# Performance work log

Hardware: AMD Instinct MI355X
Metric: run time of the kernel (lower is better)

The kernel has to match this reference:

```python
import jax, jax.numpy as jnp
import numpy as np

N_NODES = 100000
N_EDGES = 1600000
IN_DIM = 256
OUT_DIM = 64


def setup_inputs() -> dict:
    key = jax.random.key(0)
    k1, k2, k3, k4, k5 = jax.random.split(key, 5)
    x = jax.random.normal(k1, (N_NODES, IN_DIM), dtype=jnp.float32)
    # glorot-ish small scales to keep the learned power exponent well-behaved
    W = jax.random.normal(k2, (IN_DIM, OUT_DIM), dtype=jnp.float32) * 0.05
    f_w = jax.random.normal(k3, (2 * OUT_DIM, 1), dtype=jnp.float32) * 0.05
    f_b = jnp.full((1,), 0.5, dtype=jnp.float32)  # constants([1], 0.5)
    row = jax.random.randint(k4, (N_EDGES,), 0, N_NODES, dtype=jnp.int64)
    col = jax.random.randint(k5, (N_EDGES,), 0, N_NODES, dtype=jnp.int64)
    return {"x": x, "W": W, "f_w": f_w, "f_b": f_b, "row": row, "col": col}


def reference(x, W, f_w, f_b, row, col):
    n = x.shape[0]
    pre_sup = x @ W                                   # [N, out]
    vi = pre_sup[row]                                 # [E, out] gather src
    vj = pre_sup[col]                                 # [E, out] gather dst
    # tiny edge MLP: score per edge
    s = jnp.concatenate([vi, vj], axis=1) @ f_w + f_b  # [E, 1]
    # degree = adjacency row-sum including self-loop (adj + I)
    deg = jax.ops.segment_sum(jnp.ones(row.shape[0], x.dtype), row,
                              num_segments=n) + 1.0    # [N]
    deg_vivj = (deg[row] * deg[col])[:, None]          # [E, 1]
    vals = jnp.power(deg_vivj, -s)[:, 0]               # [E] edge weights
    # sparse(support) @ pre_sup  ==  scatter-add over destination rows
    out = jax.ops.segment_sum(vals[:, None] * vj, row, num_segments=n)
    return jax.nn.relu(out)
```

## Files before the change

kernel.cpp:

```cpp
#include <hip/hip_runtime.h>

#define IN_DIM 256
#define OUT_DIM 64

typedef __attribute__((ext_vector_type(8))) short short8;
typedef __attribute__((ext_vector_type(4))) float frag_cd;

__device__ __forceinline__ unsigned short bf16_rne(float f) {
    unsigned u = __float_as_uint(f);
    u = (u + 0x7FFFu + ((u >> 16) & 1u)) >> 16;
    return (unsigned short)u;
}
__device__ __forceinline__ float bf16_to_f32(unsigned short h) {
    return __uint_as_float((unsigned)h << 16);
}

__global__ __launch_bounds__(256) void wprep_kernel(const float* __restrict__ W,
                                                    const float* __restrict__ f_w,
                                                    short8* __restrict__ wfrag,
                                                    float* __restrict__ wf0,
                                                    float* __restrict__ wf1) {
    const int t = threadIdx.x;
    float s0 = 0.f, s1 = 0.f;
    #pragma unroll 8
    for (int c = 0; c < 64; c++) {
        const float w = W[t * 64 + c];
        s0 += w * f_w[c];
        s1 += w * f_w[64 + c];
    }
    wf0[t] = s0;
    wf1[t] = s1;
    for (int e = t; e < 2048; e += 256) {
        const int lane = e & 63;
        const int ct = e >> 6;
        const int chunk = ct >> 2, tile = ct & 3;
        const int kb = chunk * 32 + ((lane >> 4) * 8);
        const int n = tile * 16 + (lane & 15);
        short8 f;
        #pragma unroll
        for (int j = 0; j < 8; j++)
            f[j] = (short)bf16_rne(W[(kb + j) * 64 + n]);
        wfrag[e] = f;
    }
}

__global__ __launch_bounds__(256) void gemm_rank_kernel(const float* __restrict__ x,
                                                        const short8* __restrict__ wfrag,
                                                        const float* __restrict__ wf0,
                                                        const float* __restrict__ wf1,
                                                        unsigned short* __restrict__ pre16,
                                                        float* __restrict__ a,
                                                        float2* __restrict__ bl,
                                                        const int* __restrict__ row,
                                                        unsigned* __restrict__ cnt,
                                                        unsigned* __restrict__ rank,
                                                        int N, int E,
                                                        int nblk_gemm, int nblk_rank, int G) {
    __shared__ short8 lds_wfrag[2048];
    __shared__ float4 lds_wf0[64];
    __shared__ float4 lds_wf1[64];
    const int r4 = blockIdx.x & 3;
    const int s = blockIdx.x >> 2;
    if (r4 != 3) {
        const int rb = s * 3 + r4;
        if (rb >= nblk_rank) return;
        const int i0 = rb * 1024 + threadIdx.x;
        const int i1 = i0 + 256, i2 = i0 + 512, i3 = i0 + 768;
        const bool v0 = i0 < E, v1 = i1 < E, v2 = i2 < E, v3 = i3 < E;
        unsigned rk0 = 0, rk1 = 0, rk2 = 0, rk3 = 0;
        if (v0) rk0 = atomicAdd(&cnt[row[i0]], 1u);
        if (v1) rk1 = atomicAdd(&cnt[row[i1]], 1u);
        if (v2) rk2 = atomicAdd(&cnt[row[i2]], 1u);
        if (v3) rk3 = atomicAdd(&cnt[row[i3]], 1u);
        if (rank) {
            if (v0) rank[i0] = rk0;
            if (v1) rank[i1] = rk1;
            if (v2) rank[i2] = rk2;
            if (v3) rank[i3] = rk3;
        }
        return;
    }
    const int g = s;
    if (g >= G) return;
    const int t = threadIdx.x;
    const int w = t >> 6;
    const int l = t & 63;
    const int m = l & 15;
    const int q = l >> 4;

    #pragma unroll
    for (int e = t; e < 2048; e += 256)
        ((int4*)lds_wfrag)[e] = ((const int4*)wfrag)[e];
    if (t < 64) lds_wf0[t] = ((const float4*)wf0)[t];
    else if (t < 128) lds_wf1[t - 64] = ((const float4*)wf1)[t - 64];
    __syncthreads();

    for (int tile = g; tile < nblk_gemm; tile += G) {
        const int row0 = tile * 64 + w * 16;
        const int arow = row0 + m;
        const int arowc = (arow < N) ? arow : (N - 1);
        const float* xr = x + (size_t)arowc * IN_DIM;

        float4 xv[16];
        #pragma unroll
        for (int c = 0; c < 8; c++) {
            xv[2 * c]     = *(const float4*)&xr[c * 32 + q * 8];
            xv[2 * c + 1] = *(const float4*)&xr[c * 32 + q * 8 + 4];
        }
        __builtin_amdgcn_sched_barrier(0);

        frag_cd acc0 = {0.f, 0.f, 0.f, 0.f};
        frag_cd acc1 = acc0, acc2 = acc0, acc3 = acc0;
        float ap = 0.f, bp = 0.f;

        #pragma unroll
        for (int c = 0; c < 8; c++) {
            const int k4 = c * 8 + q * 2;
            const float4 w0l = lds_wf0[k4];
            const float4 w0h = lds_wf0[k4 + 1];
            const float4 w1l = lds_wf1[k4];
            const float4 w1h = lds_wf1[k4 + 1];
            const short8 b0 = lds_wfrag[(c * 4 + 0) * 64 + l];
            const short8 b1 = lds_wfrag[(c * 4 + 1) * 64 + l];
            const short8 b2 = lds_wfrag[(c * 4 + 2) * 64 + l];
            const short8 b3 = lds_wfrag[(c * 4 + 3) * 64 + l];
            const float4 xl = xv[2 * c];
            const float4 xh = xv[2 * c + 1];

            ap += xl.x * w0l.x + xl.y * w0l.y + xl.z * w0l.z + xl.w * w0l.w
                + xh.x * w0h.x + xh.y * w0h.y + xh.z * w0h.z + xh.w * w0h.w;
            bp += xl.x * w1l.x + xl.y * w1l.y + xl.z * w1l.z + xl.w * w1l.w
                + xh.x * w1h.x + xh.y * w1h.y + xh.z * w1h.z + xh.w * w1h.w;

            short8 a8;
            a8[0] = (short)bf16_rne(xl.x); a8[1] = (short)bf16_rne(xl.y);
            a8[2] = (short)bf16_rne(xl.z); a8[3] = (short)bf16_rne(xl.w);
            a8[4] = (short)bf16_rne(xh.x); a8[5] = (short)bf16_rne(xh.y);
            a8[6] = (short)bf16_rne(xh.z); a8[7] = (short)bf16_rne(xh.w);

            acc0 = __builtin_amdgcn_mfma_f32_16x16x32_bf16(a8, b0, acc0, 0, 0, 0);
            acc1 = __builtin_amdgcn_mfma_f32_16x16x32_bf16(a8, b1, acc1, 0, 0, 0);
            acc2 = __builtin_amdgcn_mfma_f32_16x16x32_bf16(a8, b2, acc2, 0, 0, 0);
            acc3 = __builtin_amdgcn_mfma_f32_16x16x32_bf16(a8, b3, acc3, 0, 0, 0);
        }

        ap += __shfl_xor(ap, 16, 64); ap += __shfl_xor(ap, 32, 64);
        bp += __shfl_xor(bp, 16, 64); bp += __shfl_xor(bp, 32, 64);
        if (q == 0 && arow < N) { a[arow] = ap; bl[arow].x = bp; }

        const frag_cd* accs[4] = {&acc0, &acc1, &acc2, &acc3};
        #pragma unroll
        for (int tt = 0; tt < 4; tt++) {
            #pragma unroll
            for (int r = 0; r < 4; r++) {
                const int ro = row0 + q * 4 + r;
                if (ro < N)
                    pre16[(size_t)ro * OUT_DIM + tt * 16 + m] = bf16_rne((*accs[tt])[r]);
            }
        }
    }
}

__global__ __launch_bounds__(256) void scan1_kernel(const unsigned* __restrict__ cnt,
                                                    unsigned* __restrict__ incl,
                                                    unsigned* __restrict__ bsum, int N) {
    __shared__ unsigned s[256];
    const int t = threadIdx.x;
    const int i = blockIdx.x * 256 + t;
    const unsigned v = (i < N) ? cnt[i] : 0u;
    s[t] = v; __syncthreads();
    for (int off = 1; off < 256; off <<= 1) {
        const unsigned u = (t >= off) ? s[t - off] : 0u;
        __syncthreads();
        s[t] += u;
        __syncthreads();
    }
    if (i < N) incl[i] = s[t];
    if (t == 255) bsum[blockIdx.x] = s[255];
}

__global__ __launch_bounds__(256) void scan3_kernel(unsigned* __restrict__ row_start,
                                                    const unsigned* __restrict__ cnt,
                                                    float2* __restrict__ bl,
                                                    const unsigned* __restrict__ bsum,
                                                    int N, int E) {
    __shared__ unsigned red[256];
    const int t = threadIdx.x;
    unsigned partial = 0;
    for (int k = t; k < (int)blockIdx.x; k += 256) partial += bsum[k];
    red[t] = partial; __syncthreads();
    #pragma unroll
    for (int off = 128; off > 0; off >>= 1) {
        if (t < off) red[t] += red[t + off];
        __syncthreads();
    }
    const unsigned ex0 = red[0];
    const int i = blockIdx.x * 256 + t;
    if (i >= N) return;
    const unsigned incl = row_start[i];
    const unsigned c = cnt[i];
    row_start[i] = ex0 + incl - c;
    bl[i].y = __logf((float)(c + 1u));
    if (i == N - 1) row_start[N] = (unsigned)E;
}

__global__ __launch_bounds__(256) void scatter_pos_kernel(const int* __restrict__ row,
                                                          const int* __restrict__ col,
                                                          const unsigned* __restrict__ rank,
                                                          const unsigned* __restrict__ row_start,
                                                          int* __restrict__ scol, int E) {
    const int e = blockIdx.x * blockDim.x + threadIdx.x;
    if (e < E)
        scol[row_start[row[e]] + rank[e]] = col[e];
}

__global__ __launch_bounds__(256) void accum_kernel(const unsigned short* __restrict__ pre16,
                                                    const int* __restrict__ scol,
                                                    const unsigned* __restrict__ row_start,
                                                    const float* __restrict__ a,
                                                    const float2* __restrict__ bl,
                                                    const float* __restrict__ f_b,
                                                    float* __restrict__ out, int N) {
    const int lane = threadIdx.x & 63;
    const int eo = lane >> 5;
    const int d = lane & 31;
    const int n = (int)((blockIdx.x * blockDim.x + threadIdx.x) >> 6);
    if (n >= N) return;
    const unsigned* __restrict__ pre32 = (const unsigned*)pre16;
    const unsigned s0 = row_start[n], s1 = row_start[n + 1];
    const float an = a[n] + f_b[0];
    const float ldr = bl[n].y;
    float accx = 0.f, accy = 0.f;
    unsigned j = s0;
    for (; j + 8 <= s1; j += 8) {
        const int c0 = scol[j + eo];
        const int c1 = scol[j + 2 + eo];
        const int c2 = scol[j + 4 + eo];
        const int c3 = scol[j + 6 + eo];
        const float2 o0 = bl[c0];
        const float2 o1 = bl[c1];
        const float2 o2 = bl[c2];
        const float2 o3 = bl[c3];
        const unsigned p0 = pre32[(size_t)c0 * 32 + d];
        const unsigned p1 = pre32[(size_t)c1 * 32 + d];
        const unsigned p2 = pre32[(size_t)c2 * 32 + d];
        const unsigned p3 = pre32[(size_t)c3 * 32 + d];
        const float v0 = __expf(-(an + o0.x) * (ldr + o0.y));
        const float v1 = __expf(-(an + o1.x) * (ldr + o1.y));
        const float v2 = __expf(-(an + o2.x) * (ldr + o2.y));
        const float v3 = __expf(-(an + o3.x) * (ldr + o3.y));
        accx += v0 * bf16_to_f32((unsigned short)(p0 & 0xffffu));
        accy += v0 * bf16_to_f32((unsigned short)(p0 >> 16));
        accx += v1 * bf16_to_f32((unsigned short)(p1 & 0xffffu));
        accy += v1 * bf16_to_f32((unsigned short)(p1 >> 16));
        accx += v2 * bf16_to_f32((unsigned short)(p2 & 0xffffu));
        accy += v2 * bf16_to_f32((unsigned short)(p2 >> 16));
        accx += v3 * bf16_to_f32((unsigned short)(p3 & 0xffffu));
        accy += v3 * bf16_to_f32((unsigned short)(p3 >> 16));
    }
    for (; j + 4 <= s1; j += 4) {
        const int c0 = scol[j + eo];
        const int c1 = scol[j + 2 + eo];
        const float2 o0 = bl[c0];
        const float2 o1 = bl[c1];
        const unsigned p0 = pre32[(size_t)c0 * 32 + d];
        const unsigned p1 = pre32[(size_t)c1 * 32 + d];
        const float v0 = __expf(-(an + o0.x) * (ldr + o0.y));
        const float v1 = __expf(-(an + o1.x) * (ldr + o1.y));
        accx += v0 * bf16_to_f32((unsigned short)(p0 & 0xffffu));
        accy += v0 * bf16_to_f32((unsigned short)(p0 >> 16));
        accx += v1 * bf16_to_f32((unsigned short)(p1 & 0xffffu));
        accy += v1 * bf16_to_f32((unsigned short)(p1 >> 16));
    }
    if (j + 2 <= s1) {
        const int c0 = scol[j + eo];
        const float2 o0 = bl[c0];
        const unsigned p0 = pre32[(size_t)c0 * 32 + d];
        const float v0 = __expf(-(an + o0.x) * (ldr + o0.y));
        accx += v0 * bf16_to_f32((unsigned short)(p0 & 0xffffu));
        accy += v0 * bf16_to_f32((unsigned short)(p0 >> 16));
        j += 2;
    }
    if (j < s1 && eo == 0) {
        const int c0 = scol[j];
        const float2 o0 = bl[c0];
        const unsigned p0 = pre32[(size_t)c0 * 32 + d];
        const float v0 = __expf(-(an + o0.x) * (ldr + o0.y));
        accx += v0 * bf16_to_f32((unsigned short)(p0 & 0xffffu));
        accy += v0 * bf16_to_f32((unsigned short)(p0 >> 16));
    }
    accx += __shfl_xor(accx, 32, 64);
    accy += __shfl_xor(accy, 32, 64);
    if (eo == 0) {
        const float2 o = make_float2(fmaxf(accx, 0.f), fmaxf(accy, 0.f));
        *(float2*)&out[(size_t)n * 64 + 2 * d] = o;
    }
}

__global__ __launch_bounds__(256) void edge_atomic_kernel(const unsigned short* __restrict__ pre16,
                                                          const float* __restrict__ a,
                                                          const float2* __restrict__ bl,
                                                          const float* __restrict__ f_b,
                                                          const int* __restrict__ row,
                                                          const int* __restrict__ col,
                                                          float* __restrict__ out, int E) {
    const int lane = threadIdx.x & 63;
    const int wave = (int)((blockIdx.x * blockDim.x + threadIdx.x) >> 6);
    const int nwaves = (int)((gridDim.x * blockDim.x) >> 6);
    const float fb = f_b[0];
    for (int e = wave; e < E; e += nwaves) {
        const int r = row[e];
        const int c = col[e];
        const float s = a[r] + bl[c].x + fb;
        const float val = __expf(-s * (bl[r].y + bl[c].y));
        atomicAdd(&out[(size_t)r * 64 + lane],
                  val * bf16_to_f32(pre16[(size_t)c * 64 + lane]));
    }
}

__global__ __launch_bounds__(256) void relu_kernel(float4* __restrict__ out, int n4) {
    const int i = blockIdx.x * blockDim.x + threadIdx.x;
    if (i < n4) {
        float4 v = out[i];
        v.x = fmaxf(v.x, 0.f); v.y = fmaxf(v.y, 0.f);
        v.z = fmaxf(v.z, 0.f); v.w = fmaxf(v.w, 0.f);
        out[i] = v;
    }
}

extern "C" void kernel_launch(void* const* d_in, const int* in_sizes, int n_in,
                              void* d_out, int out_size, void* d_ws, size_t ws_size,
                              hipStream_t stream) {
    const float* x   = (const float*)d_in[0];
    const float* W   = (const float*)d_in[1];
    const float* f_w = (const float*)d_in[2];
    const float* f_b = (const float*)d_in[3];
    const int*   row = (const int*)d_in[4];
    const int*   col = (const int*)d_in[5];
    float* out = (float*)d_out;

    const int N = in_sizes[0] / IN_DIM;
    const int E = in_sizes[4];

    size_t off = 0;
    auto salloc = [&](size_t bytes) { size_t p = off; off = (off + bytes + 255) & ~(size_t)255; return p; };
    char* w8 = (char*)d_ws;
    unsigned short* pre16 = (unsigned short*)(w8 + salloc((size_t)N * OUT_DIM * sizeof(unsigned short)));
    unsigned* row_start = (unsigned*)(w8 + salloc((size_t)(N + 1) * sizeof(unsigned)));
    unsigned* cnt       = (unsigned*)(w8 + salloc((size_t)N * sizeof(unsigned)));
    float*    a         = (float*)   (w8 + salloc((size_t)N * sizeof(float)));
    float2*   bl        = (float2*)  (w8 + salloc((size_t)N * sizeof(float2)));
    unsigned* bsum      = (unsigned*)(w8 + salloc(512 * sizeof(unsigned)));
    short8*   wfrag     = (short8*)  (w8 + salloc(2048 * sizeof(short8)));
    float*    wf0       = (float*)   (w8 + salloc(256 * sizeof(float)));
    float*    wf1       = (float*)   (w8 + salloc(256 * sizeof(float)));
    int*      scol      = (int*)     (w8 + salloc((size_t)E * sizeof(int)));
    unsigned* rank      = (unsigned*)(w8 + salloc((size_t)E * sizeof(unsigned)));
    const size_t need_full = off;

    const int nb = (N + 255) / 256;
    const int nblk_gemm = (N + 63) / 64;
    const int nblk_node = (N + 3) / 4;
    const int nblk_edge = (E + 255) / 256;
    const int nblk_rank = (E + 1023) / 1024;
    const int G = (nblk_gemm < 512) ? nblk_gemm : 512;
    const int stripes = (((nblk_rank + 2) / 3) > G) ? ((nblk_rank + 2) / 3) : G;
    const int nblk_fused = stripes * 4;

    hipMemsetAsync(cnt, 0, (size_t)N * sizeof(unsigned), stream);
    wprep_kernel<<<1, 256, 0, stream>>>(W, f_w, wfrag, wf0, wf1);

    if (need_full <= ws_size) {
        gemm_rank_kernel<<<nblk_fused, 256, 0, stream>>>(x, wfrag, wf0, wf1, pre16, a, bl,
                                                         row, cnt, rank, N, E,
                                                         nblk_gemm, nblk_rank, G);
        scan1_kernel<<<nb, 256, 0, stream>>>(cnt, row_start, bsum, N);
        scan3_kernel<<<nb, 256, 0, stream>>>(row_start, cnt, bl, bsum, N, E);
        scatter_pos_kernel<<<nblk_edge, 256, 0, stream>>>(row, col, rank, row_start, scol, E);
        accum_kernel<<<nblk_node, 256, 0, stream>>>(pre16, scol, row_start, a, bl, f_b, out, N);
    } else {
        gemm_rank_kernel<<<nblk_fused, 256, 0, stream>>>(x, wfrag, wf0, wf1, pre16, a, bl,
                                                         row, cnt, (unsigned*)nullptr, N, E,
                                                         nblk_gemm, nblk_rank, G);
        scan1_kernel<<<nb, 256, 0, stream>>>(cnt, row_start, bsum, N);
        scan3_kernel<<<nb, 256, 0, stream>>>(row_start, cnt, bl, bsum, N, E);
        hipMemsetAsync(out, 0, (size_t)out_size * sizeof(float), stream);
        edge_atomic_kernel<<<4096, 256, 0, stream>>>(pre16, a, bl, f_b, row, col, out, E);
        const int n4 = out_size / 4;
        relu_kernel<<<(n4 + 255) / 256, 256, 0, stream>>>((float4*)out, n4);
    }
}
```

Measured before the change: 342.0 us.

## Fuse GEMM tile and edge histogram slice into every block

Changes the fused GEMM+rank kernel from specialised blocks (three rank blocks for every persistent GEMM block, with a grid-stride tile loop) to one GEMM tile per block, followed in the same block by a contiguous slice of edge-degree atomics. x loads are now issued before the LDS weight staging, so the global loads overlap the LDS fill. The aim is to balance the memory-bound GEMM with the atomic histogram inside each block and to remove the persistent loop. The cost is that every block reloads the weight fragments into LDS (about 1563 blocks instead of 512) and runs its atomics only after its GEMM tile finishes.

```diff
diff --git a/kernel.cpp b/kernel.cpp
--- a/kernel.cpp
+++ b/kernel.cpp
@@ -55,48 +55,19 @@
                                                         unsigned* __restrict__ cnt,
                                                         unsigned* __restrict__ rank,
                                                         int N, int E,
-                                                        int nblk_gemm, int nblk_rank, int G) {
+                                                        int nblk_gemm, int EPB) {
     __shared__ short8 lds_wfrag[2048];
     __shared__ float4 lds_wf0[64];
     __shared__ float4 lds_wf1[64];
-    const int r4 = blockIdx.x & 3;
-    const int s = blockIdx.x >> 2;
-    if (r4 != 3) {
-        const int rb = s * 3 + r4;
-        if (rb >= nblk_rank) return;
-        const int i0 = rb * 1024 + threadIdx.x;
-        const int i1 = i0 + 256, i2 = i0 + 512, i3 = i0 + 768;
-        const bool v0 = i0 < E, v1 = i1 < E, v2 = i2 < E, v3 = i3 < E;
-        unsigned rk0 = 0, rk1 = 0, rk2 = 0, rk3 = 0;
-        if (v0) rk0 = atomicAdd(&cnt[row[i0]], 1u);
-        if (v1) rk1 = atomicAdd(&cnt[row[i1]], 1u);
-        if (v2) rk2 = atomicAdd(&cnt[row[i2]], 1u);
-        if (v3) rk3 = atomicAdd(&cnt[row[i3]], 1u);
-        if (rank) {
-            if (v0) rank[i0] = rk0;
-            if (v1) rank[i1] = rk1;
-            if (v2) rank[i2] = rk2;
-            if (v3) rank[i3] = rk3;
-        }
-        return;
-    }
-    const int g = s;
-    if (g >= G) return;
+    const int b = blockIdx.x;
     const int t = threadIdx.x;
-    const int w = t >> 6;
-    const int l = t & 63;
-    const int m = l & 15;
-    const int q = l >> 4;
-
-    #pragma unroll
-    for (int e = t; e < 2048; e += 256)
-        ((int4*)lds_wfrag)[e] = ((const int4*)wfrag)[e];
-    if (t < 64) lds_wf0[t] = ((const float4*)wf0)[t];
-    else if (t < 128) lds_wf1[t - 64] = ((const float4*)wf1)[t - 64];
-    __syncthreads();
-
-    for (int tile = g; tile < nblk_gemm; tile += G) {
-        const int row0 = tile * 64 + w * 16;
+
+    if (b < nblk_gemm) {
+        const int w = t >> 6;
+        const int l = t & 63;
+        const int m = l & 15;
+        const int q = l >> 4;
+        const int row0 = b * 64 + w * 16;
         const int arow = row0 + m;
         const int arowc = (arow < N) ? arow : (N - 1);
         const float* xr = x + (size_t)arowc * IN_DIM;
@@ -107,7 +78,12 @@
             xv[2 * c]     = *(const float4*)&xr[c * 32 + q * 8];
             xv[2 * c + 1] = *(const float4*)&xr[c * 32 + q * 8 + 4];
         }
-        __builtin_amdgcn_sched_barrier(0);
+        #pragma unroll
+        for (int e = t; e < 2048; e += 256)
+            ((int4*)lds_wfrag)[e] = ((const int4*)wfrag)[e];
+        if (t < 64) lds_wf0[t] = ((const float4*)wf0)[t];
+        else if (t < 128) lds_wf1[t - 64] = ((const float4*)wf1)[t - 64];
+        __syncthreads();
 
         frag_cd acc0 = {0.f, 0.f, 0.f, 0.f};
         frag_cd acc1 = acc0, acc2 = acc0, acc3 = acc0;
@@ -157,6 +133,31 @@
                 if (ro < N)
                     pre16[(size_t)ro * OUT_DIM + tt * 16 + m] = bf16_rne((*accs[tt])[r]);
             }
+        }
+    }
+
+    const int estart = b * EPB;
+    const int elim0 = estart + EPB;
+    const int elim = (elim0 < E) ? elim0 : E;
+    for (int base = estart; base < elim; base += 1024) {
+        const int i0 = base + t;
+        const int i1 = i0 + 256, i2 = i0 + 512, i3 = i0 + 768;
+        const bool v0 = i0 < elim, v1 = i1 < elim, v2 = i2 < elim, v3 = i3 < elim;
+        int r0 = 0, r1 = 0, r2 = 0, r3 = 0;
+        if (v0) r0 = row[i0];
+        if (v1) r1 = row[i1];
+        if (v2) r2 = row[i2];
+        if (v3) r3 = row[i3];
+        unsigned rk0 = 0, rk1 = 0, rk2 = 0, rk3 = 0;
+        if (v0) rk0 = atomicAdd(&cnt[r0], 1u);
+        if (v1) rk1 = atomicAdd(&cnt[r1], 1u);
+        if (v2) rk2 = atomicAdd(&cnt[r2], 1u);
+        if (v3) rk3 = atomicAdd(&cnt[r3], 1u);
+        if (rank) {
+            if (v0) rank[i0] = rk0;
+            if (v1) rank[i1] = rk1;
+            if (v2) rank[i2] = rk2;
+            if (v3) rank[i3] = rk3;
         }
     }
 }
@@ -362,10 +363,10 @@
     const int nblk_gemm = (N + 63) / 64;
     const int nblk_node = (N + 3) / 4;
     const int nblk_edge = (E + 255) / 256;
-    const int nblk_rank = (E + 1023) / 1024;
-    const int G = (nblk_gemm < 512) ? nblk_gemm : 512;
-    const int stripes = (((nblk_rank + 2) / 3) > G) ? ((nblk_rank + 2) / 3) : G;
-    const int nblk_fused = stripes * 4;
+    int EPB = (E + nblk_gemm - 1) / nblk_gemm;
+    EPB = (EPB + 255) & ~255;
+    const int nblk_hist = (E + EPB - 1) / EPB;
+    const int nblk_fused = (nblk_gemm > nblk_hist) ? nblk_gemm : nblk_hist;
 
     hipMemsetAsync(cnt, 0, (size_t)N * sizeof(unsigned), stream);
     wprep_kernel<<<1, 256, 0, stream>>>(W, f_w, wfrag, wf0, wf1);
@@ -373,7 +374,7 @@
     if (need_full <= ws_size) {
         gemm_rank_kernel<<<nblk_fused, 256, 0, stream>>>(x, wfrag, wf0, wf1, pre16, a, bl,
                                                          row, cnt, rank, N, E,
-                                                         nblk_gemm, nblk_rank, G);
+                                                         nblk_gemm, EPB);
         scan1_kernel<<<nb, 256, 0, stream>>>(cnt, row_start, bsum, N);
         scan3_kernel<<<nb, 256, 0, stream>>>(row_start, cnt, bl, bsum, N, E);
         scatter_pos_kernel<<<nblk_edge, 256, 0, stream>>>(row, col, rank, row_start, scol, E);
@@ -381,7 +382,7 @@
     } else {
         gemm_rank_kernel<<<nblk_fused, 256, 0, stream>>>(x, wfrag, wf0, wf1, pre16, a, bl,
                                                          row, cnt, (unsigned*)nullptr, N, E,
-                                                         nblk_gemm, nblk_rank, G);
+                                                         nblk_gemm, EPB);
         scan1_kernel<<<nb, 256, 0, stream>>>(cnt, row_start, bsum, N);
         scan3_kernel<<<nb, 256, 0, stream>>>(row_start, cnt, bl, bsum, N, E);
         hipMemsetAsync(out, 0, (size_t)out_size * sizeof(float), stream);
```

Result: faster. 330.6 us (-3.3%).

## Build CSR with atomic cursor scatter instead of per-edge rank array

Applied to the files above, without the earlier changes.

The degree-count pass no longer records each edge's atomic return value into a rank array. Instead scan3 initialises a per-row cursor from the exclusive prefix, and the scatter kernel claims slots with atomicAdd on that cursor. This drops an E-sized write and read, but adds a second round of E atomics. The fused GEMM/count kernel also changes from persistent strided GEMM blocks with a 3:1 interleave to one GEMM tile per block with a 4:1 interleave of one-edge-per-thread count blocks, and the x loads are issued before the LDS weight fill.

```diff
diff --git a/kernel.cpp b/kernel.cpp
--- a/kernel.cpp
+++ b/kernel.cpp
@@ -53,41 +53,37 @@
                                                         float2* __restrict__ bl,
                                                         const int* __restrict__ row,
                                                         unsigned* __restrict__ cnt,
-                                                        unsigned* __restrict__ rank,
                                                         int N, int E,
-                                                        int nblk_gemm, int nblk_rank, int G) {
+                                                        int nblk_gemm, int nblk_rank) {
     __shared__ short8 lds_wfrag[2048];
     __shared__ float4 lds_wf0[64];
     __shared__ float4 lds_wf1[64];
-    const int r4 = blockIdx.x & 3;
-    const int s = blockIdx.x >> 2;
-    if (r4 != 3) {
-        const int rb = s * 3 + r4;
+    const int s = blockIdx.x / 5;
+    const int r5 = blockIdx.x % 5;
+    if (r5 != 4) {
+        const int rb = s * 4 + r5;
         if (rb >= nblk_rank) return;
-        const int i0 = rb * 1024 + threadIdx.x;
-        const int i1 = i0 + 256, i2 = i0 + 512, i3 = i0 + 768;
-        const bool v0 = i0 < E, v1 = i1 < E, v2 = i2 < E, v3 = i3 < E;
-        unsigned rk0 = 0, rk1 = 0, rk2 = 0, rk3 = 0;
-        if (v0) rk0 = atomicAdd(&cnt[row[i0]], 1u);
-        if (v1) rk1 = atomicAdd(&cnt[row[i1]], 1u);
-        if (v2) rk2 = atomicAdd(&cnt[row[i2]], 1u);
-        if (v3) rk3 = atomicAdd(&cnt[row[i3]], 1u);
-        if (rank) {
-            if (v0) rank[i0] = rk0;
-            if (v1) rank[i1] = rk1;
-            if (v2) rank[i2] = rk2;
-            if (v3) rank[i3] = rk3;
-        }
+        const int i = rb * 256 + threadIdx.x;
+        if (i < E) atomicAdd(&cnt[row[i]], 1u);
         return;
     }
-    const int g = s;
-    if (g >= G) return;
+    if (s >= nblk_gemm) return;
     const int t = threadIdx.x;
     const int w = t >> 6;
     const int l = t & 63;
     const int m = l & 15;
     const int q = l >> 4;
-
+    const int row0 = s * 64 + w * 16;
+    const int arow = row0 + m;
+    const int arowc = (arow < N) ? arow : (N - 1);
+    const float* xr = x + (size_t)arowc * IN_DIM;
+
+    float4 xv[16];
+    #pragma unroll
+    for (int c = 0; c < 8; c++) {
+        xv[2 * c]     = *(const float4*)&xr[c * 32 + q * 8];
+        xv[2 * c + 1] = *(const float4*)&xr[c * 32 + q * 8 + 4];
+    }
     #pragma unroll
     for (int e = t; e < 2048; e += 256)
         ((int4*)lds_wfrag)[e] = ((const int4*)wfrag)[e];
@@ -95,68 +91,53 @@
     else if (t < 128) lds_wf1[t - 64] = ((const float4*)wf1)[t - 64];
     __syncthreads();
 
-    for (int tile = g; tile < nblk_gemm; tile += G) {
-        const int row0 = tile * 64 + w * 16;
-        const int arow = row0 + m;
-        const int arowc = (arow < N) ? arow : (N - 1);
-        const float* xr = x + (size_t)arowc * IN_DIM;
-
-        float4 xv[16];
+    frag_cd acc0 = {0.f, 0.f, 0.f, 0.f};
+    frag_cd acc1 = acc0, acc2 = acc0, acc3 = acc0;
+    float ap = 0.f, bp = 0.f;
+
+    #pragma unroll
+    for (int c = 0; c < 8; c++) {
+        const int k4 = c * 8 + q * 2;
+        const float4 w0l = lds_wf0[k4];
+        const float4 w0h = lds_wf0[k4 + 1];
+        const float4 w1l = lds_wf1[k4];
+        const float4 w1h = lds_wf1[k4 + 1];
+        const short8 b0 = lds_wfrag[(c * 4 + 0) * 64 + l];
+        const short8 b1 = lds_wfrag[(c * 4 + 1) * 64 + l];
+        const short8 b2 = lds_wfrag[(c * 4 + 2) * 64 + l];
+        const short8 b3 = lds_wfrag[(c * 4 + 3) * 64 + l];
+        const float4 xl = xv[2 * c];
+        const float4 xh = xv[2 * c + 1];
+
+        ap += xl.x * w0l.x + xl.y * w0l.y + xl.z * w0l.z + xl.w * w0l.w
+            + xh.x * w0h.x + xh.y * w0h.y + xh.z * w0h.z + xh.w * w0h.w;
+        bp += xl.x * w1l.x + xl.y * w1l.y + xl.z * w1l.z + xl.w * w1l.w
+            + xh.x * w1h.x + xh.y * w1h.y + xh.z * w1h.z + xh.w * w1h.w;
+
+        short8 a8;
+        a8[0] = (short)bf16_rne(xl.x); a8[1] = (short)bf16_rne(xl.y);
+        a8[2] = (short)bf16_rne(xl.z); a8[3] = (short)bf16_rne(xl.w);
+        a8[4] = (short)bf16_rne(xh.x); a8[5] = (short)bf16_rne(xh.y);
+        a8[6] = (short)bf16_rne(xh.z); a8[7] = (short)bf16_rne(xh.w);
+
+        acc0 = __builtin_amdgcn_mfma_f32_16x16x32_bf16(a8, b0, acc0, 0, 0, 0);
+        acc1 = __builtin_amdgcn_mfma_f32_16x16x32_bf16(a8, b1, acc1, 0, 0, 0);
+        acc2 = __builtin_amdgcn_mfma_f32_16x16x32_bf16(a8, b2, acc2, 0, 0, 0);
+        acc3 = __builtin_amdgcn_mfma_f32_16x16x32_bf16(a8, b3, acc3, 0, 0, 0);
+    }
+
+    ap += __shfl_xor(ap, 16, 64); ap += __shfl_xor(ap, 32, 64);
+    bp += __shfl_xor(bp, 16, 64); bp += __shfl_xor(bp, 32, 64);
+    if (q == 0 && arow < N) { a[arow] = ap; bl[arow].x = bp; }
+
+    const frag_cd* accs[4] = {&acc0, &acc1, &acc2, &acc3};
+    #pragma unroll
+    for (int tt = 0; tt < 4; tt++) {
         #pragma unroll
-        for (int c = 0; c < 8; c++) {
-            xv[2 * c]     = *(const float4*)&xr[c * 32 + q * 8];
-            xv[2 * c + 1] = *(const float4*)&xr[c * 32 + q * 8 + 4];
-        }
-        __builtin_amdgcn_sched_barrier(0);
-
-        frag_cd acc0 = {0.f, 0.f, 0.f, 0.f};
-        frag_cd acc1 = acc0, acc2 = acc0, acc3 = acc0;
-        float ap = 0.f, bp = 0.f;
-
-        #pragma unroll
-        for (int c = 0; c < 8; c++) {
-            const int k4 = c * 8 + q * 2;
-            const float4 w0l = lds_wf0[k4];
-            const float4 w0h = lds_wf0[k4 + 1];
-            const float4 w1l = lds_wf1[k4];
-            const float4 w1h = lds_wf1[k4 + 1];
-            const short8 b0 = lds_wfrag[(c * 4 + 0) * 64 + l];
-            const short8 b1 = lds_wfrag[(c * 4 + 1) * 64 + l];
-            const short8 b2 = lds_wfrag[(c * 4 + 2) * 64 + l];
-            const short8 b3 = lds_wfrag[(c * 4 + 3) * 64 + l];
-            const float4 xl = xv[2 * c];
-            const float4 xh = xv[2 * c + 1];
-
-            ap += xl.x * w0l.x + xl.y * w0l.y + xl.z * w0l.z + xl.w * w0l.w
-                + xh.x * w0h.x + xh.y * w0h.y + xh.z * w0h.z + xh.w * w0h.w;
-            bp += xl.x * w1l.x + xl.y * w1l.y + xl.z * w1l.z + xl.w * w1l.w
-                + xh.x * w1h.x + xh.y * w1h.y + xh.z * w1h.z + xh.w * w1h.w;
-
-            short8 a8;
-            a8[0] = (short)bf16_rne(xl.x); a8[1] = (short)bf16_rne(xl.y);
-            a8[2] = (short)bf16_rne(xl.z); a8[3] = (short)bf16_rne(xl.w);
-            a8[4] = (short)bf16_rne(xh.x); a8[5] = (short)bf16_rne(xh.y);
-            a8[6] = (short)bf16_rne(xh.z); a8[7] = (short)bf16_rne(xh.w);
-
-            acc0 = __builtin_amdgcn_mfma_f32_16x16x32_bf16(a8, b0, acc0, 0, 0, 0);
-            acc1 = __builtin_amdgcn_mfma_f32_16x16x32_bf16(a8, b1, acc1, 0, 0, 0);
-            acc2 = __builtin_amdgcn_mfma_f32_16x16x32_bf16(a8, b2, acc2, 0, 0, 0);
-            acc3 = __builtin_amdgcn_mfma_f32_16x16x32_bf16(a8, b3, acc3, 0, 0, 0);
-        }
-
-        ap += __shfl_xor(ap, 16, 64); ap += __shfl_xor(ap, 32, 64);
-        bp += __shfl_xor(bp, 16, 64); bp += __shfl_xor(bp, 32, 64);
-        if (q == 0 && arow < N) { a[arow] = ap; bl[arow].x = bp; }
-
-        const frag_cd* accs[4] = {&acc0, &acc1, &acc2, &acc3};
-        #pragma unroll
-        for (int tt = 0; tt < 4; tt++) {
-            #pragma unroll
-            for (int r = 0; r < 4; r++) {
-                const int ro = row0 + q * 4 + r;
-                if (ro < N)
-                    pre16[(size_t)ro * OUT_DIM + tt * 16 + m] = bf16_rne((*accs[tt])[r]);
-            }
+        for (int r = 0; r < 4; r++) {
+            const int ro = row0 + q * 4 + r;
+            if (ro < N)
+                pre16[(size_t)ro * OUT_DIM + tt * 16 + m] = bf16_rne((*accs[tt])[r]);
         }
     }
 }
@@ -181,6 +162,7 @@
 
 __global__ __launch_bounds__(256) void scan3_kernel(unsigned* __restrict__ row_start,
                                                     const unsigned* __restrict__ cnt,
+                                                    unsigned* __restrict__ cursor,
                                                     float2* __restrict__ bl,
                                                     const unsigned* __restrict__ bsum,
                                                     int N, int E) {
@@ -199,19 +181,36 @@
     if (i >= N) return;
     const unsigned incl = row_start[i];
     const unsigned c = cnt[i];
-    row_start[i] = ex0 + incl - c;
+    const unsigned ex = ex0 + incl - c;
+    row_start[i] = ex;
+    cursor[i] = ex;
     bl[i].y = __logf((float)(c + 1u));
     if (i == N - 1) row_start[N] = (unsigned)E;
 }
 
 __global__ __launch_bounds__(256) void scatter_pos_kernel(const int* __restrict__ row,
                                                           const int* __restrict__ col,
-                                                          const unsigned* __restrict__ rank,
-                                                          const unsigned* __restrict__ row_start,
+                                                          unsigned* __restrict__ cursor,
                                                           int* __restrict__ scol, int E) {
-    const int e = blockIdx.x * blockDim.x + threadIdx.x;
-    if (e < E)
-        scol[row_start[row[e]] + rank[e]] = col[e];
+    const int t = threadIdx.x;
+    const int i0 = blockIdx.x * 1024 + t;
+    const int i1 = i0 + 256, i2 = i0 + 512, i3 = i0 + 768;
+    const bool v0 = i0 < E, v1 = i1 < E, v2 = i2 < E, v3 = i3 < E;
+    int r0 = 0, r1 = 0, r2 = 0, r3 = 0;
+    int c0 = 0, c1 = 0, c2 = 0, c3 = 0;
+    if (v0) { r0 = row[i0]; c0 = col[i0]; }
+    if (v1) { r1 = row[i1]; c1 = col[i1]; }
+    if (v2) { r2 = row[i2]; c2 = col[i2]; }
+    if (v3) { r3 = row[i3]; c3 = col[i3]; }
+    unsigned k0 = 0, k1 = 0, k2 = 0, k3 = 0;
+    if (v0) k0 = atomicAdd(&cursor[r0], 1u);
+    if (v1) k1 = atomicAdd(&cursor[r1], 1u);
+    if (v2) k2 = atomicAdd(&cursor[r2], 1u);
+    if (v3) k3 = atomicAdd(&cursor[r3], 1u);
+    if (v0) scol[k0] = c0;
+    if (v1) scol[k1] = c1;
+    if (v2) scol[k2] = c2;
+    if (v3) scol[k3] = c3;
 }
 
 __global__ __launch_bounds__(256) void accum_kernel(const unsigned short* __restrict__ pre16,
@@ -348,6 +347,7 @@
     unsigned short* pre16 = (unsigned short*)(w8 + salloc((size_t)N * OUT_DIM * sizeof(unsigned short)));
     unsigned* row_start = (unsigned*)(w8 + salloc((size_t)(N + 1) * sizeof(unsigned)));
     unsigned* cnt       = (unsigned*)(w8 + salloc((size_t)N * sizeof(unsigned)));
+    unsigned* cursor    = (unsigned*)(w8 + salloc((size_t)N * sizeof(unsigned)));
     float*    a         = (float*)   (w8 + salloc((size_t)N * sizeof(float)));
     float2*   bl        = (float2*)  (w8 + salloc((size_t)N * sizeof(float2)));
     unsigned* bsum      = (unsigned*)(w8 + salloc(512 * sizeof(unsigned)));
@@ -355,35 +355,33 @@
     float*    wf0       = (float*)   (w8 + salloc(256 * sizeof(float)));
     float*    wf1       = (float*)   (w8 + salloc(256 * sizeof(float)));
     int*      scol      = (int*)     (w8 + salloc((size_t)E * sizeof(int)));
-    unsigned* rank      = (unsigned*)(w8 + salloc((size_t)E * sizeof(unsigned)));
     const size_t need_full = off;
 
     const int nb = (N + 255) / 256;
     const int nblk_gemm = (N + 63) / 64;
     const int nblk_node = (N + 3) / 4;
     const int nblk_edge = (E + 255) / 256;
-    const int nblk_rank = (E + 1023) / 1024;
-    const int G = (nblk_gemm < 512) ? nblk_gemm : 512;
-    const int stripes = (((nblk_rank + 2) / 3) > G) ? ((nblk_rank + 2) / 3) : G;
-    const int nblk_fused = stripes * 4;
+    const int nblk_scat = (E + 1023) / 1024;
+    const int stripes = (((nblk_edge + 3) / 4) > nblk_gemm) ? ((nblk_edge + 3) / 4) : nblk_gemm;
+    const int nblk_fused = stripes * 5;
 
     hipMemsetAsync(cnt, 0, (size_t)N * sizeof(unsigned), stream);
     wprep_kernel<<<1, 256, 0, stream>>>(W, f_w, wfrag, wf0, wf1);
 
     if (need_full <= ws_size) {
         gemm_rank_kernel<<<nblk_fused, 256, 0, stream>>>(x, wfrag, wf0, wf1, pre16, a, bl,
-                                                         row, cnt, rank, N, E,
-                                                         nblk_gemm, nblk_rank, G);
+                                                         row, cnt, N, E,
+                                                         nblk_gemm, nblk_edge);
         scan1_kernel<<<nb, 256, 0, stream>>>(cnt, row_start, bsum, N);
-        scan3_kernel<<<nb, 256, 0, stream>>>(row_start, cnt, bl, bsum, N, E);
-        scatter_pos_kernel<<<nblk_edge, 256, 0, stream>>>(row, col, rank, row_start, scol, E);
+        scan3_kernel<<<nb, 256, 0, stream>>>(row_start, cnt, cursor, bl, bsum, N, E);
+        scatter_pos_kernel<<<nblk_scat, 256, 0, stream>>>(row, col, cursor, scol, E);
         accum_kernel<<<nblk_node, 256, 0, stream>>>(pre16, scol, row_start, a, bl, f_b, out, N);
     } else {
         gemm_rank_kernel<<<nblk_fused, 256, 0, stream>>>(x, wfrag, wf0, wf1, pre16, a, bl,
-                                                         row, cnt, (unsigned*)nullptr, N, E,
-                                                         nblk_gemm, nblk_rank, G);
+                                                         row, cnt, N, E,
+                                                         nblk_gemm, nblk_edge);
         scan1_kernel<<<nb, 256, 0, stream>>>(cnt, row_start, bsum, N);
-        scan3_kernel<<<nb, 256, 0, stream>>>(row_start, cnt, bl, bsum, N, E);
+        scan3_kernel<<<nb, 256, 0, stream>>>(row_start, cnt, cursor, bl, bsum, N, E);
         hipMemsetAsync(out, 0, (size_t)out_size * sizeof(float), stream);
         edge_atomic_kernel<<<4096, 256, 0, stream>>>(pre16, a, bl, f_b, row, col, out, E);
         const int n4 = out_size / 4;
```

Measured after the change: 389.2 us. 13.8% more time.

## Use one tile per GEMM block and one edge per thread in fused rank kernel

Applied to the files above, without the earlier changes.

The fused GEMM+rank kernel moves from a persistent grid-stride GEMM loop (capped at 512 blocks) with 4-edges-per-thread rank blocks to one 64-row tile per GEMM block and one edge per thread, interleaved 4 rank blocks per GEMM block. The x loads are now issued before the LDS weight staging so global latency overlaps the weight copy. The aim is more parallelism and better load overlap. The cost is many more blocks, each reloading the 32KB weight fragment into LDS, and fewer atomics in flight per thread.

```diff
diff --git a/kernel.cpp b/kernel.cpp
--- a/kernel.cpp
+++ b/kernel.cpp
@@ -55,39 +55,39 @@
                                                         unsigned* __restrict__ cnt,
                                                         unsigned* __restrict__ rank,
                                                         int N, int E,
-                                                        int nblk_gemm, int nblk_rank, int G) {
+                                                        int nblk_gemm, int nblk_rank) {
     __shared__ short8 lds_wfrag[2048];
     __shared__ float4 lds_wf0[64];
     __shared__ float4 lds_wf1[64];
-    const int r4 = blockIdx.x & 3;
-    const int s = blockIdx.x >> 2;
-    if (r4 != 3) {
-        const int rb = s * 3 + r4;
+    const int s = blockIdx.x / 5;
+    const int r5 = blockIdx.x % 5;
+    if (r5 != 4) {
+        const int rb = s * 4 + r5;
         if (rb >= nblk_rank) return;
-        const int i0 = rb * 1024 + threadIdx.x;
-        const int i1 = i0 + 256, i2 = i0 + 512, i3 = i0 + 768;
-        const bool v0 = i0 < E, v1 = i1 < E, v2 = i2 < E, v3 = i3 < E;
-        unsigned rk0 = 0, rk1 = 0, rk2 = 0, rk3 = 0;
-        if (v0) rk0 = atomicAdd(&cnt[row[i0]], 1u);
-        if (v1) rk1 = atomicAdd(&cnt[row[i1]], 1u);
-        if (v2) rk2 = atomicAdd(&cnt[row[i2]], 1u);
-        if (v3) rk3 = atomicAdd(&cnt[row[i3]], 1u);
-        if (rank) {
-            if (v0) rank[i0] = rk0;
-            if (v1) rank[i1] = rk1;
-            if (v2) rank[i2] = rk2;
-            if (v3) rank[i3] = rk3;
+        const int i = rb * 256 + threadIdx.x;
+        if (i < E) {
+            const unsigned rk = atomicAdd(&cnt[row[i]], 1u);
+            if (rank) rank[i] = rk;
         }
         return;
     }
-    const int g = s;
-    if (g >= G) return;
+    if (s >= nblk_gemm) return;
     const int t = threadIdx.x;
     const int w = t >> 6;
     const int l = t & 63;
     const int m = l & 15;
     const int q = l >> 4;
-
+    const int row0 = s * 64 + w * 16;
+    const int arow = row0 + m;
+    const int arowc = (arow < N) ? arow : (N - 1);
+    const float* xr = x + (size_t)arowc * IN_DIM;
+
+    float4 xv[16];
+    #pragma unroll
+    for (int c = 0; c < 8; c++) {
+        xv[2 * c]     = *(const float4*)&xr[c * 32 + q * 8];
+        xv[2 * c + 1] = *(const float4*)&xr[c * 32 + q * 8 + 4];
+    }
     #pragma unroll
     for (int e = t; e < 2048; e += 256)
         ((int4*)lds_wfrag)[e] = ((const int4*)wfrag)[e];
@@ -95,68 +95,53 @@
     else if (t < 128) lds_wf1[t - 64] = ((const float4*)wf1)[t - 64];
     __syncthreads();
 
-    for (int tile = g; tile < nblk_gemm; tile += G) {
-        const int row0 = tile * 64 + w * 16;
-        const int arow = row0 + m;
-        const int arowc = (arow < N) ? arow : (N - 1);
-        const float* xr = x + (size_t)arowc * IN_DIM;
-
-        float4 xv[16];
+    frag_cd acc0 = {0.f, 0.f, 0.f, 0.f};
+    frag_cd acc1 = acc0, acc2 = acc0, acc3 = acc0;
+    float ap = 0.f, bp = 0.f;
+
+    #pragma unroll
+    for (int c = 0; c < 8; c++) {
+        const int k4 = c * 8 + q * 2;
+        const float4 w0l = lds_wf0[k4];
+        const float4 w0h = lds_wf0[k4 + 1];
+        const float4 w1l = lds_wf1[k4];
+        const float4 w1h = lds_wf1[k4 + 1];
+        const short8 b0 = lds_wfrag[(c * 4 + 0) * 64 + l];
+        const short8 b1 = lds_wfrag[(c * 4 + 1) * 64 + l];
+        const short8 b2 = lds_wfrag[(c * 4 + 2) * 64 + l];
+        const short8 b3 = lds_wfrag[(c * 4 + 3) * 64 + l];
+        const float4 xl = xv[2 * c];
+        const float4 xh = xv[2 * c + 1];
+
+        ap += xl.x * w0l.x + xl.y * w0l.y + xl.z * w0l.z + xl.w * w0l.w
+            + xh.x * w0h.x + xh.y * w0h.y + xh.z * w0h.z + xh.w * w0h.w;
+        bp += xl.x * w1l.x + xl.y * w1l.y + xl.z * w1l.z + xl.w * w1l.w
+            + xh.x * w1h.x + xh.y * w1h.y + xh.z * w1h.z + xh.w * w1h.w;
+
+        short8 a8;
+        a8[0] = (short)bf16_rne(xl.x); a8[1] = (short)bf16_rne(xl.y);
+        a8[2] = (short)bf16_rne(xl.z); a8[3] = (short)bf16_rne(xl.w);
+        a8[4] = (short)bf16_rne(xh.x); a8[5] = (short)bf16_rne(xh.y);
+        a8[6] = (short)bf16_rne(xh.z); a8[7] = (short)bf16_rne(xh.w);
+
+        acc0 = __builtin_amdgcn_mfma_f32_16x16x32_bf16(a8, b0, acc0, 0, 0, 0);
+        acc1 = __builtin_amdgcn_mfma_f32_16x16x32_bf16(a8, b1, acc1, 0, 0, 0);
+        acc2 = __builtin_amdgcn_mfma_f32_16x16x32_bf16(a8, b2, acc2, 0, 0, 0);
+        acc3 = __builtin_amdgcn_mfma_f32_16x16x32_bf16(a8, b3, acc3, 0, 0, 0);
+    }
+
+    ap += __shfl_xor(ap, 16, 64); ap += __shfl_xor(ap, 32, 64);
+    bp += __shfl_xor(bp, 16, 64); bp += __shfl_xor(bp, 32, 64);
+    if (q == 0 && arow < N) { a[arow] = ap; bl[arow].x = bp; }
+
+    const frag_cd* accs[4] = {&acc0, &acc1, &acc2, &acc3};
+    #pragma unroll
+    for (int tt = 0; tt < 4; tt++) {
         #pragma unroll
-        for (int c = 0; c < 8; c++) {
-            xv[2 * c]     = *(const float4*)&xr[c * 32 + q * 8];
-            xv[2 * c + 1] = *(const float4*)&xr[c * 32 + q * 8 + 4];
-        }
-        __builtin_amdgcn_sched_barrier(0);
-
-        frag_cd acc0 = {0.f, 0.f, 0.f, 0.f};
-        frag_cd acc1 = acc0, acc2 = acc0, acc3 = acc0;
-        float ap = 0.f, bp = 0.f;
-
-        #pragma unroll
-        for (int c = 0; c < 8; c++) {
-            const int k4 = c * 8 + q * 2;
-            const float4 w0l = lds_wf0[k4];
-            const float4 w0h = lds_wf0[k4 + 1];
-            const float4 w1l = lds_wf1[k4];
-            const float4 w1h = lds_wf1[k4 + 1];
-            const short8 b0 = lds_wfrag[(c * 4 + 0) * 64 + l];
-            const short8 b1 = lds_wfrag[(c * 4 + 1) * 64 + l];
-            const short8 b2 = lds_wfrag[(c * 4 + 2) * 64 + l];
-            const short8 b3 = lds_wfrag[(c * 4 + 3) * 64 + l];
-            const float4 xl = xv[2 * c];
-            const float4 xh = xv[2 * c + 1];
-
-            ap += xl.x * w0l.x + xl.y * w0l.y + xl.z * w0l.z + xl.w * w0l.w
-                + xh.x * w0h.x + xh.y * w0h.y + xh.z * w0h.z + xh.w * w0h.w;
-            bp += xl.x * w1l.x + xl.y * w1l.y + xl.z * w1l.z + xl.w * w1l.w
-                + xh.x * w1h.x + xh.y * w1h.y + xh.z * w1h.z + xh.w * w1h.w;
-
-            short8 a8;
-            a8[0] = (short)bf16_rne(xl.x); a8[1] = (short)bf16_rne(xl.y);
-            a8[2] = (short)bf16_rne(xl.z); a8[3] = (short)bf16_rne(xl.w);
-            a8[4] = (short)bf16_rne(xh.x); a8[5] = (short)bf16_rne(xh.y);
-            a8[6] = (short)bf16_rne(xh.z); a8[7] = (short)bf16_rne(xh.w);
-
-            acc0 = __builtin_amdgcn_mfma_f32_16x16x32_bf16(a8, b0, acc0, 0, 0, 0);
-            acc1 = __builtin_amdgcn_mfma_f32_16x16x32_bf16(a8, b1, acc1, 0, 0, 0);
-            acc2 = __builtin_amdgcn_mfma_f32_16x16x32_bf16(a8, b2, acc2, 0, 0, 0);
-            acc3 = __builtin_amdgcn_mfma_f32_16x16x32_bf16(a8, b3, acc3, 0, 0, 0);
-        }
-
-        ap += __shfl_xor(ap, 16, 64); ap += __shfl_xor(ap, 32, 64);
-        bp += __shfl_xor(bp, 16, 64); bp += __shfl_xor(bp, 32, 64);
-        if (q == 0 && arow < N) { a[arow] = ap; bl[arow].x = bp; }
-
-        const frag_cd* accs[4] = {&acc0, &acc1, &acc2, &acc3};
-        #pragma unroll
-        for (int tt = 0; tt < 4; tt++) {
-            #pragma unroll
-            for (int r = 0; r < 4; r++) {
-                const int ro = row0 + q * 4 + r;
-                if (ro < N)
-                    pre16[(size_t)ro * OUT_DIM + tt * 16 + m] = bf16_rne((*accs[tt])[r]);
-            }
+        for (int r = 0; r < 4; r++) {
+            const int ro = row0 + q * 4 + r;
+            if (ro < N)
+                pre16[(size_t)ro * OUT_DIM + tt * 16 + m] = bf16_rne((*accs[tt])[r]);
         }
     }
 }
@@ -362,10 +347,8 @@
     const int nblk_gemm = (N + 63) / 64;
     const int nblk_node = (N + 3) / 4;
     const int nblk_edge = (E + 255) / 256;
-    const int nblk_rank = (E + 1023) / 1024;
-    const int G = (nblk_gemm < 512) ? nblk_gemm : 512;
-    const int stripes = (((nblk_rank + 2) / 3) > G) ? ((nblk_rank + 2) / 3) : G;
-    const int nblk_fused = stripes * 4;
+    const int stripes = (((nblk_edge + 3) / 4) > nblk_gemm) ? ((nblk_edge + 3) / 4) : nblk_gemm;
+    const int nblk_fused = stripes * 5;
 
     hipMemsetAsync(cnt, 0, (size_t)N * sizeof(unsigned), stream);
     wprep_kernel<<<1, 256, 0, stream>>>(W, f_w, wfrag, wf0, wf1);
@@ -373,7 +356,7 @@
     if (need_full <= ws_size) {
         gemm_rank_kernel<<<nblk_fused, 256, 0, stream>>>(x, wfrag, wf0, wf1, pre16, a, bl,
                                                          row, cnt, rank, N, E,
-                                                         nblk_gemm, nblk_rank, G);
+                                                         nblk_gemm, nblk_edge);
         scan1_kernel<<<nb, 256, 0, stream>>>(cnt, row_start, bsum, N);
         scan3_kernel<<<nb, 256, 0, stream>>>(row_start, cnt, bl, bsum, N, E);
         scatter_pos_kernel<<<nblk_edge, 256, 0, stream>>>(row, col, rank, row_start, scol, E);
@@ -381,7 +364,7 @@
     } else {
         gemm_rank_kernel<<<nblk_fused, 256, 0, stream>>>(x, wfrag, wf0, wf1, pre16, a, bl,
                                                          row, cnt, (unsigned*)nullptr, N, E,
-                                                         nblk_gemm, nblk_rank, G);
+                                                         nblk_gemm, nblk_edge);
         scan1_kernel<<<nb, 256, 0, stream>>>(cnt, row_start, bsum, N);
         scan3_kernel<<<nb, 256, 0, stream>>>(row_start, cnt, bl, bsum, N, E);
         hipMemsetAsync(out, 0, (size_t)out_size * sizeof(float), stream);
```

After: 313.9 us. 8.2% less time.
